# Optimization experiments

Measured on AMD Instinct MI355X. Metric: run time of the kernel, lower is better.

Reference implementation:

```python
import jax, jax.numpy as jnp
import numpy as np
from functools import partial

V, D, H, FF, NL, NC = 32000, 768, 12, 3072, 6, 1
B, L = 8, 512
EPS = 1e-5


def _layer_norm(x, g, b):
    m = jnp.mean(x, axis=-1, keepdims=True)
    v = jnp.mean((x - m) ** 2, axis=-1, keepdims=True)
    return (x - m) * jax.lax.rsqrt(v + EPS) * g + b


def setup_inputs() -> dict:
    key = jax.random.key(0)
    ks = jax.random.split(key, 24)
    s = 0.02
    inp = {
        'x': jax.random.randint(ks[0], (B, L), 0, V),
        'mask': jnp.ones((B, L), dtype=jnp.int32),
        'emb': jax.random.normal(ks[1], (V, D), jnp.float32) * s,
        # per-layer stacked params, leading dim = NL (scanned over)
        'Wq': jax.random.normal(ks[2], (NL, D, D), jnp.float32) * s,
        'bq': jnp.zeros((NL, D), jnp.float32),
        'Wk': jax.random.normal(ks[3], (NL, D, D), jnp.float32) * s,
        'bk': jnp.zeros((NL, D), jnp.float32),
        'Wv': jax.random.normal(ks[4], (NL, D, D), jnp.float32) * s,
        'bv': jnp.zeros((NL, D), jnp.float32),
        'Wo': jax.random.normal(ks[5], (NL, D, D), jnp.float32) * s,
        'bo': jnp.zeros((NL, D), jnp.float32),
        'W1': jax.random.normal(ks[6], (NL, D, FF), jnp.float32) * s,
        'b1': jnp.zeros((NL, FF), jnp.float32),
        'W2': jax.random.normal(ks[7], (NL, FF, D), jnp.float32) * s,
        'b2': jnp.zeros((NL, D), jnp.float32),
        'g1': jnp.ones((NL, D), jnp.float32),
        'be1': jnp.zeros((NL, D), jnp.float32),
        'g2': jnp.ones((NL, D), jnp.float32),
        'be2': jnp.zeros((NL, D), jnp.float32),
        'Wc': jax.random.normal(ks[8], (D, NC), jnp.float32) * s,
        'bc': jnp.zeros((NC,), jnp.float32),
    }
    return inp


def _forward(x, mask, emb, Wq, bq, Wk, bk, Wv, bv, Wo, bo, W1, b1, W2, b2,
             g1, be1, g2, be2, Wc, bc):
    Bx, Lx = x.shape
    Dm = emb.shape[1]
    dh = Dm // H
    scale = jnp.float32(np.sqrt(Dm / H))

    h = emb[x]  # [B,L,D]

    # PositionalEncoding (faithful to original buggy broadcast: pe[:B,0,:] added per-batch)
    pos = jnp.arange(Bx, dtype=jnp.float32)[:, None]
    div = jnp.exp(jnp.arange(0, Dm, 2, dtype=jnp.float32) * (-np.log(10000.0) / Dm))
    pe = jnp.stack([jnp.sin(pos * div), jnp.cos(pos * div)], axis=-1).reshape(Bx, Dm)
    h = h + pe[:, None, :]

    t = jnp.arange(Lx, dtype=jnp.float32)
    bias = -0.01 * (t[:, None] - t[None, :])  # [L,L]
    mask_b = (mask == 0)[:, None, None, :]    # [B,1,1,L]

    def step(h, p):
        (wq, bq_, wk, bk_, wv, bv_, wo, bo_, w1, b1_, w2, b2_,
         g1_, be1_, g2_, be2_) = p
        xn = _layer_norm(h, g1_, be1_)
        Q = (xn @ wq + bq_).reshape(Bx, Lx, H, dh)
        K = (xn @ wk + bk_).reshape(Bx, Lx, H, dh)
        Vv = (xn @ wv + bv_).reshape(Bx, Lx, H, dh)
        scores = jnp.einsum('bqhd,bkhd->bhqk', Q, K) / scale + bias
        scores = jnp.where(mask_b, -jnp.inf, scores)
        attn = jax.nn.softmax(scores, axis=-1)  # [B,H,L,L]
        out = jnp.einsum('bhqk,bkhd->bqhd', attn, Vv).reshape(Bx, Lx, Dm)
        h = h + (out @ wo + bo_)
        xn2 = _layer_norm(h, g2_, be2_)
        ff = jax.nn.gelu(xn2 @ w1 + b1_, approximate=False) @ w2 + b2_
        h = h + ff
        return h, attn

    params = (Wq, bq, Wk, bk, Wv, bv, Wo, bo, W1, b1, W2, b2, g1, be1, g2, be2)
    h, attn_all = jax.lax.scan(step, h, params)  # attn_all: [NL,B,H,L,L]
    logits = h[:, 0, :] @ Wc + bc  # CLS token -> [B,NC]
    return logits, attn_all


def reference(x, mask, emb, Wq, bq, Wk, bk, Wv, bv, Wo, bo, W1, b1, W2, b2,
              g1, be1, g2, be2, Wc, bc):
    return _forward(x, mask, emb, Wq, bq, Wk, bk, Wv, bv, Wo, bo,
                    W1, b1, W2, b2, g1, be1, g2, be2, Wc, bc)
```

## Files before the change

kernel.cpp:

```cpp
#include <hip/hip_runtime.h>
#include <math.h>

#define DMODEL 768
#define SEQL   512
#define NBATCH 8
#define NHEAD  12
#define NLAYER 6
#define FFDIM  3072
#define DHEAD  64
#define ROWS   (NBATCH * SEQL)
#define ATTN_PER_LAYER ((size_t)NBATCH * NHEAD * SEQL * SEQL)

using f32x4 = __attribute__((ext_vector_type(4))) float;
using f16x8 = __attribute__((ext_vector_type(8))) _Float16;
using f16x4 = __attribute__((ext_vector_type(4))) _Float16;

__device__ __forceinline__ void gload16(const void* g, void* l) {
    __builtin_amdgcn_global_load_lds(
        (const __attribute__((address_space(1))) unsigned int*)g,
        (__attribute__((address_space(3))) unsigned int*)l, 16, 0, 0);
}

__global__ __launch_bounds__(256) void embed_kernel(const int* __restrict__ x,
                                                    const float* __restrict__ emb,
                                                    float* __restrict__ h) {
    int bl = blockIdx.x;
    int b = bl >> 9;
    int tok = x[bl];
    const float* e = emb + (size_t)tok * DMODEL;
    float* hp = h + (size_t)bl * DMODEL;
    const float c = -0.011992632f;
#pragma unroll
    for (int u = 0; u < 3; ++u) {
        int d = threadIdx.x + u * 256;
        int i = d >> 1;
        float div = expf((float)(2 * i) * c);
        float ang = (float)b * div;
        float pe = (d & 1) ? cosf(ang) : sinf(ang);
        hp[d] = e[d] + pe;
    }
}

__global__ __launch_bounds__(256) void ln_kernel(const float* __restrict__ X,
                                                 const float* __restrict__ g,
                                                 const float* __restrict__ be,
                                                 _Float16* __restrict__ Yh,
                                                 _Float16* __restrict__ Yl) {
    int row = blockIdx.x;
    const float* x = X + (size_t)row * DMODEL;
    size_t base = (size_t)row * DMODEL;
    int t = threadIdx.x;
    float v0 = x[t], v1 = x[t + 256], v2 = x[t + 512];
    float s = v0 + v1 + v2;
    __shared__ float sb[8];
    for (int off = 32; off; off >>= 1) s += __shfl_down(s, off, 64);
    int lane = t & 63, wid = t >> 6;
    if (!lane) sb[wid] = s;
    __syncthreads();
    float mean = (sb[0] + sb[1] + sb[2] + sb[3]) * (1.0f / DMODEL);
    float d0 = v0 - mean, d1 = v1 - mean, d2 = v2 - mean;
    float q = d0 * d0 + d1 * d1 + d2 * d2;
    for (int off = 32; off; off >>= 1) q += __shfl_down(q, off, 64);
    if (!lane) sb[4 + wid] = q;
    __syncthreads();
    float var = (sb[4] + sb[5] + sb[6] + sb[7]) * (1.0f / DMODEL);
    float inv = 1.0f / sqrtf(var + 1e-5f);
    float y0 = d0 * inv * g[t] + be[t];
    float y1 = d1 * inv * g[t + 256] + be[t + 256];
    float y2 = d2 * inv * g[t + 512] + be[t + 512];
    _Float16 h0 = (_Float16)y0, h1 = (_Float16)y1, h2 = (_Float16)y2;
    Yh[base + t] = h0;       Yl[base + t] = (_Float16)(y0 - (float)h0);
    Yh[base + t + 256] = h1; Yl[base + t + 256] = (_Float16)(y1 - (float)h1);
    Yh[base + t + 512] = h2; Yl[base + t + 512] = (_Float16)(y2 - (float)h2);
}

__global__ __launch_bounds__(256) void wconv_kernel(const float* __restrict__ W,
                                                    _Float16* __restrict__ Th,
                                                    _Float16* __restrict__ Tl,
                                                    int K, int N) {
    __shared__ float t[32][33];
    int n0 = blockIdx.x * 32, k0 = blockIdx.y * 32;
    int tx = threadIdx.x & 31, ty = threadIdx.x >> 5;
#pragma unroll
    for (int u = 0; u < 4; ++u)
        t[ty + u * 8][tx] = W[(size_t)(k0 + ty + u * 8) * N + n0 + tx];
    __syncthreads();
#pragma unroll
    for (int u = 0; u < 4; ++u) {
        int r = ty + u * 8;
        float v = t[tx][r];
        _Float16 hi = (_Float16)v;
        size_t o = (size_t)(n0 + r) * K + k0 + tx;
        Th[o] = hi;
        Tl[o] = (_Float16)(v - (float)hi);
    }
}

__global__ __launch_bounds__(256) void fconv_kernel(const float* __restrict__ X,
                                                    _Float16* __restrict__ Xh,
                                                    _Float16* __restrict__ Xl,
                                                    int n4) {
    int i = blockIdx.x * 256 + threadIdx.x;
    if (i >= n4) return;
    float4 v = ((const float4*)X)[i];
    f16x4 hh, ll;
    hh[0] = (_Float16)v.x; ll[0] = (_Float16)(v.x - (float)hh[0]);
    hh[1] = (_Float16)v.y; ll[1] = (_Float16)(v.y - (float)hh[1]);
    hh[2] = (_Float16)v.z; ll[2] = (_Float16)(v.z - (float)hh[2]);
    hh[3] = (_Float16)v.w; ll[3] = (_Float16)(v.w - (float)hh[3]);
    ((f16x4*)Xh)[i] = hh;
    ((f16x4*)Xl)[i] = ll;
}

__global__ __launch_bounds__(256) void bcat_kernel(const float* __restrict__ a,
                                                   const float* __restrict__ b,
                                                   const float* __restrict__ c,
                                                   float* __restrict__ o) {
    int t = blockIdx.x * 256 + threadIdx.x;
    o[t] = (t < DMODEL) ? a[t] : (t < 2 * DMODEL ? b[t - DMODEL] : c[t - 2 * DMODEL]);
}

__global__ __launch_bounds__(256) void mgemm_kernel(
    const _Float16* __restrict__ Ah, const _Float16* __restrict__ Al,
    const _Float16* __restrict__ Bh, const _Float16* __restrict__ Bl,
    const float* __restrict__ bias, float* __restrict__ C,
    _Float16* __restrict__ Ch, _Float16* __restrict__ Cl,
    int N, int K, int flags) {
    __shared__ __attribute__((aligned(16))) _Float16 Ash[128][32];
    __shared__ __attribute__((aligned(16))) _Float16 Asl[128][32];
    __shared__ __attribute__((aligned(16))) _Float16 Bsh[128][32];
    __shared__ __attribute__((aligned(16))) _Float16 Bsl[128][32];

    int tid = threadIdx.x;
    int w = tid >> 6, lane = tid & 63;
    int m0 = blockIdx.y * 128, n0 = blockIdx.x * 128;
    int kper = K / gridDim.z;
    int kbeg = blockIdx.z * kper;

    int srow = lane >> 2;
    int kch = (lane & 3) ^ ((lane >> 3) & 3);
    size_t aoff0 = (size_t)(m0 + w * 16 + srow) * K + kch * 8;
    size_t aoff1 = (size_t)(m0 + (w + 4) * 16 + srow) * K + kch * 8;
    size_t boff0 = (size_t)(n0 + w * 16 + srow) * K + kch * 8;
    size_t boff1 = (size_t)(n0 + (w + 4) * 16 + srow) * K + kch * 8;
    _Float16* lAh0 = &Ash[w * 16][0];
    _Float16* lAh1 = &Ash[(w + 4) * 16][0];
    _Float16* lAl0 = &Asl[w * 16][0];
    _Float16* lAl1 = &Asl[(w + 4) * 16][0];
    _Float16* lBh0 = &Bsh[w * 16][0];
    _Float16* lBh1 = &Bsh[(w + 4) * 16][0];
    _Float16* lBl0 = &Bsl[w * 16][0];
    _Float16* lBl1 = &Bsl[(w + 4) * 16][0];

    int fr = lane & 15, kg = lane >> 4;
    int kb = (kg ^ ((fr >> 1) & 3)) * 8;
    int wr = w >> 1, wc = w & 1;

    f32x4 acc[4][4];
#pragma unroll
    for (int i = 0; i < 4; ++i)
#pragma unroll
        for (int j = 0; j < 4; ++j)
#pragma unroll
            for (int r = 0; r < 4; ++r) acc[i][j][r] = 0.0f;

    for (int k0 = kbeg; k0 < kbeg + kper; k0 += 32) {
        gload16(Ah + aoff0 + k0, lAh0);
        gload16(Ah + aoff1 + k0, lAh1);
        gload16(Al + aoff0 + k0, lAl0);
        gload16(Al + aoff1 + k0, lAl1);
        gload16(Bh + boff0 + k0, lBh0);
        gload16(Bh + boff1 + k0, lBh1);
        gload16(Bl + boff0 + k0, lBl0);
        gload16(Bl + boff1 + k0, lBl1);
        asm volatile("s_waitcnt vmcnt(0)" ::: "memory");
        __syncthreads();

        f16x8 a_h[4], a_l[4], b_h[4], b_l[4];
#pragma unroll
        for (int i = 0; i < 4; ++i) {
            int r = wr * 64 + i * 16 + fr;
            a_h[i] = *(const f16x8*)&Ash[r][kb];
            a_l[i] = *(const f16x8*)&Asl[r][kb];
        }
#pragma unroll
        for (int j = 0; j < 4; ++j) {
            int r = wc * 64 + j * 16 + fr;
            b_h[j] = *(const f16x8*)&Bsh[r][kb];
            b_l[j] = *(const f16x8*)&Bsl[r][kb];
        }
#pragma unroll
        for (int i = 0; i < 4; ++i)
#pragma unroll
            for (int j = 0; j < 4; ++j) {
                acc[i][j] = __builtin_amdgcn_mfma_f32_16x16x32_f16(a_h[i], b_h[j], acc[i][j], 0, 0, 0);
                acc[i][j] = __builtin_amdgcn_mfma_f32_16x16x32_f16(a_h[i], b_l[j], acc[i][j], 0, 0, 0);
                acc[i][j] = __builtin_amdgcn_mfma_f32_16x16x32_f16(a_l[i], b_h[j], acc[i][j], 0, 0, 0);
            }
        __syncthreads();
    }

    int od = kg * 4;
#pragma unroll
    for (int j = 0; j < 4; ++j) {
        int col = n0 + wc * 64 + j * 16 + fr;
        float bv = (bias && blockIdx.z == 0) ? bias[col] : 0.0f;
#pragma unroll
        for (int i = 0; i < 4; ++i) {
#pragma unroll
            for (int r = 0; r < 4; ++r) {
                int rowg = m0 + wr * 64 + i * 16 + od + r;
                float v = acc[i][j][r] + bv;
                if (flags & 1) v = 0.5f * v * (1.0f + erff(v * 0.70710678118654752f));
                size_t o = (size_t)rowg * N + col;
                if (flags & 4) {
                    _Float16 hv = (_Float16)v;
                    Ch[o] = hv;
                    Cl[o] = (_Float16)(v - (float)hv);
                } else if (flags & 2) {
                    unsafeAtomicAdd(&C[o], v);
                } else {
                    C[o] = v;
                }
            }
        }
    }
}

__global__ __launch_bounds__(256) void gemm_kernel(
    const float* __restrict__ A, const float* __restrict__ W,
    const float* __restrict__ bias, float* __restrict__ C,
    int M, int N, int K, int lda, int ldw, int ldc,
    int zmod, long long sAb, long long sAh, long long sWb, long long sWh,
    long long sCb, long long sCh, int flags) {
    int z = blockIdx.z;
    int zb = z / zmod, zh = z % zmod;
    A += zb * sAb + zh * sAh;
    W += zb * sWb + zh * sWh;
    C += zb * sCb + zh * sCh;

    __shared__ float As[16][65];
    __shared__ float Bs[16][64];
    int m0 = blockIdx.y * 64, n0 = blockIdx.x * 64;
    int tid = threadIdx.x;
    int tx = tid & 15, ty = tid >> 4;
    int arow = tid >> 2;
    int akk  = (tid & 3) << 2;
    int bkk  = tid >> 4;
    int bnn  = (tid & 15) << 2;
    float acc[4][4] = {};

    for (int k0 = 0; k0 < K; k0 += 16) {
        float4 av = *(const float4*)(A + (size_t)(m0 + arow) * lda + k0 + akk);
        float4 wv = *(const float4*)(W + (size_t)(k0 + bkk) * ldw + n0 + bnn);
        As[akk + 0][arow] = av.x;
        As[akk + 1][arow] = av.y;
        As[akk + 2][arow] = av.z;
        As[akk + 3][arow] = av.w;
        *(float4*)&Bs[bkk][bnn] = wv;
        __syncthreads();
#pragma unroll
        for (int k = 0; k < 16; ++k) {
            float a[4], bb[4];
#pragma unroll
            for (int i = 0; i < 4; ++i) a[i] = As[k][ty * 4 + i];
#pragma unroll
            for (int j = 0; j < 4; ++j) bb[j] = Bs[k][tx * 4 + j];
#pragma unroll
            for (int i = 0; i < 4; ++i)
#pragma unroll
                for (int j = 0; j < 4; ++j) acc[i][j] = fmaf(a[i], bb[j], acc[i][j]);
        }
        __syncthreads();
    }

#pragma unroll
    for (int i = 0; i < 4; ++i) {
        size_t rbase = (size_t)(m0 + ty * 4 + i) * ldc;
#pragma unroll
        for (int j = 0; j < 4; ++j) {
            int col = n0 + tx * 4 + j;
            float v = acc[i][j] + (bias ? bias[col] : 0.0f);
            if (flags & 1) v = 0.5f * v * (1.0f + erff(v * 0.70710678118654752f));
            if (flags & 2) C[rbase + col] += v;
            else           C[rbase + col] = v;
        }
    }
}

__global__ __launch_bounds__(256) void scores_kernel(const float* __restrict__ Q,
                                                     const float* __restrict__ Kmat,
                                                     const int* __restrict__ mask,
                                                     float* __restrict__ P,
                                                     int ldq) {
    int kt = blockIdx.x, qt = blockIdx.y, bh = blockIdx.z;
    int b = bh / NHEAD, hh = bh % NHEAD;
    int q0 = qt * 64, k0 = kt * 32;
    __shared__ float Qs[64][65];
    __shared__ float Ks[32][65];
    const float* Qg = Q + ((size_t)(b * SEQL + q0)) * ldq + hh * DHEAD;
    const float* Kg = Kmat + ((size_t)(b * SEQL + k0)) * ldq + hh * DHEAD;
    {
        int r = threadIdx.x >> 2;
        int c0 = (threadIdx.x & 3) * 16;
#pragma unroll
        for (int u = 0; u < 4; ++u) {
            float4 v = *(const float4*)(Qg + (size_t)r * ldq + c0 + u * 4);
            Qs[r][c0 + u * 4 + 0] = v.x;
            Qs[r][c0 + u * 4 + 1] = v.y;
            Qs[r][c0 + u * 4 + 2] = v.z;
            Qs[r][c0 + u * 4 + 3] = v.w;
        }
    }
    {
        int r = threadIdx.x >> 3;
        int c0 = (threadIdx.x & 7) * 8;
#pragma unroll
        for (int u = 0; u < 2; ++u) {
            float4 v = *(const float4*)(Kg + (size_t)r * ldq + c0 + u * 4);
            Ks[r][c0 + u * 4 + 0] = v.x;
            Ks[r][c0 + u * 4 + 1] = v.y;
            Ks[r][c0 + u * 4 + 2] = v.z;
            Ks[r][c0 + u * 4 + 3] = v.w;
        }
    }
    __syncthreads();
    int tq = threadIdx.x >> 3;
    int tk = threadIdx.x & 7;
    float acc[2][4] = {};
#pragma unroll 8
    for (int d = 0; d < 64; ++d) {
        float qa0 = Qs[tq * 2 + 0][d];
        float qa1 = Qs[tq * 2 + 1][d];
#pragma unroll
        for (int j = 0; j < 4; ++j) {
            float kb2 = Ks[tk * 4 + j][d];
            acc[0][j] = fmaf(qa0, kb2, acc[0][j]);
            acc[1][j] = fmaf(qa1, kb2, acc[1][j]);
        }
    }
    size_t pbase = ((size_t)(b * NHEAD + hh)) * SEQL;
#pragma unroll
    for (int i = 0; i < 2; ++i) {
        int qg = q0 + tq * 2 + i;
#pragma unroll
        for (int j = 0; j < 4; ++j) {
            int kg2 = k0 + tk * 4 + j;
            float v = acc[i][j] * 0.125f - 0.01f * ((float)qg - (float)kg2);
            if (mask[b * SEQL + kg2] == 0) v = -INFINITY;
            P[(pbase + qg) * SEQL + kg2] = v;
        }
    }
}

__global__ __launch_bounds__(256) void softmax_kernel(float* __restrict__ P) {
    int row = blockIdx.x * 4 + (threadIdx.x >> 6);
    int lane = threadIdx.x & 63;
    float* p = P + (size_t)row * SEQL;
    float v[8];
#pragma unroll
    for (int j = 0; j < 8; ++j) v[j] = p[lane + 64 * j];
    float m = v[0];
#pragma unroll
    for (int j = 1; j < 8; ++j) m = fmaxf(m, v[j]);
    for (int off = 32; off; off >>= 1) m = fmaxf(m, __shfl_xor(m, off, 64));
    float s = 0.0f;
#pragma unroll
    for (int j = 0; j < 8; ++j) {
        v[j] = expf(v[j] - m);
        s += v[j];
    }
    for (int off = 32; off; off >>= 1) s += __shfl_xor(s, off, 64);
    float inv = 1.0f / s;
#pragma unroll
    for (int j = 0; j < 8; ++j) p[lane + 64 * j] = v[j] * inv;
}

__global__ __launch_bounds__(256) void logits_kernel(const float* __restrict__ h,
                                                     const float* __restrict__ Wc,
                                                     const float* __restrict__ bc,
                                                     float* __restrict__ out) {
    int b = blockIdx.x;
    const float* hp = h + (size_t)b * SEQL * DMODEL;
    int t = threadIdx.x;
    float s = hp[t] * Wc[t] + hp[t + 256] * Wc[t + 256] + hp[t + 512] * Wc[t + 512];
    __shared__ float sb[4];
    for (int off = 32; off; off >>= 1) s += __shfl_down(s, off, 64);
    int lane = t & 63, wid = t >> 6;
    if (!lane) sb[wid] = s;
    __syncthreads();
    if (t == 0) out[b] = sb[0] + sb[1] + sb[2] + sb[3] + bc[0];
}

extern "C" void kernel_launch(void* const* d_in, const int* in_sizes, int n_in,
                              void* d_out, int out_size, void* d_ws, size_t ws_size,
                              hipStream_t stream) {
    (void)in_sizes; (void)n_in; (void)out_size; (void)ws_size;
    const int*   x    = (const int*)d_in[0];
    const int*   mask = (const int*)d_in[1];
    const float* emb  = (const float*)d_in[2];
    const float* Wq   = (const float*)d_in[3];
    const float* bq   = (const float*)d_in[4];
    const float* Wk   = (const float*)d_in[5];
    const float* bk   = (const float*)d_in[6];
    const float* Wv   = (const float*)d_in[7];
    const float* bv   = (const float*)d_in[8];
    const float* Wo   = (const float*)d_in[9];
    const float* bo   = (const float*)d_in[10];
    const float* W1   = (const float*)d_in[11];
    const float* b1   = (const float*)d_in[12];
    const float* W2   = (const float*)d_in[13];
    const float* b2   = (const float*)d_in[14];
    const float* g1   = (const float*)d_in[15];
    const float* be1  = (const float*)d_in[16];
    const float* g2   = (const float*)d_in[17];
    const float* be2  = (const float*)d_in[18];
    const float* Wc   = (const float*)d_in[19];
    const float* bc   = (const float*)d_in[20];

    float* out  = (float*)d_out;
    float* attn = out + NBATCH * 1;

    const size_t RD  = (size_t)ROWS * DMODEL;
    const size_t RFF = (size_t)ROWS * FFDIM;
    const size_t DD  = (size_t)DMODEL * DMODEL;
    const size_t DF  = (size_t)DMODEL * FFDIM;

    float* ws   = (float*)d_ws;
    float* h    = ws;
    float* qkvb = h + RD;
    float* att  = qkvb + 3 * RD;
    _Float16* xnh  = (_Float16*)(att + RD);
    _Float16* xnl  = xnh + RD;
    _Float16* atth = xnl + RD;
    _Float16* attl = atth + RD;
    _Float16* ffh  = attl + RD;
    _Float16* ffl  = ffh + RFF;
    _Float16* wqkvh = ffl + RFF;
    _Float16* wqkvl = wqkvh + 3 * DD;
    _Float16* woh  = wqkvl + 3 * DD;
    _Float16* wol  = woh + DD;
    _Float16* w1h  = wol + DD;
    _Float16* w1l  = w1h + DF;
    _Float16* w2h  = w1l + DF;
    _Float16* w2l  = w2h + DF;
    float* bqkv = (float*)(w2l + DF);

    embed_kernel<<<ROWS, 256, 0, stream>>>(x, emb, h);

    for (int l = 0; l < NLAYER; ++l) {
        const float* wq = Wq + (size_t)l * DD;
        const float* wk = Wk + (size_t)l * DD;
        const float* wv = Wv + (size_t)l * DD;
        const float* wo = Wo + (size_t)l * DD;
        const float* w1 = W1 + (size_t)l * DF;
        const float* w2 = W2 + (size_t)l * DF;
        float* P = attn + (size_t)l * ATTN_PER_LAYER;

        wconv_kernel<<<dim3(24, 24), 256, 0, stream>>>(wq, wqkvh,          wqkvl,          DMODEL, DMODEL);
        wconv_kernel<<<dim3(24, 24), 256, 0, stream>>>(wk, wqkvh + DD,     wqkvl + DD,     DMODEL, DMODEL);
        wconv_kernel<<<dim3(24, 24), 256, 0, stream>>>(wv, wqkvh + 2 * DD, wqkvl + 2 * DD, DMODEL, DMODEL);
        wconv_kernel<<<dim3(24, 24), 256, 0, stream>>>(wo, woh, wol, DMODEL, DMODEL);
        wconv_kernel<<<dim3(96, 24), 256, 0, stream>>>(w1, w1h, w1l, DMODEL, FFDIM);
        wconv_kernel<<<dim3(24, 96), 256, 0, stream>>>(w2, w2h, w2l, FFDIM, DMODEL);
        bcat_kernel<<<9, 256, 0, stream>>>(bq + l * DMODEL, bk + l * DMODEL, bv + l * DMODEL, bqkv);

        ln_kernel<<<ROWS, 256, 0, stream>>>(h, g1 + l * DMODEL, be1 + l * DMODEL, xnh, xnl);

        mgemm_kernel<<<dim3(18, 32, 1), 256, 0, stream>>>(
            xnh, xnl, wqkvh, wqkvl, bqkv, qkvb, nullptr, nullptr,
            3 * DMODEL, DMODEL, 0);

        scores_kernel<<<dim3(SEQL / 32, SEQL / 64, NBATCH * NHEAD), 256, 0, stream>>>(
            qkvb, qkvb + DMODEL, mask, P, 3 * DMODEL);
        softmax_kernel<<<(NBATCH * NHEAD * SEQL) / 4, 256, 0, stream>>>(P);

        gemm_kernel<<<dim3(1, SEQL / 64, NBATCH * NHEAD), 256, 0, stream>>>(
            P, qkvb + 2 * DMODEL, nullptr, att,
            SEQL, DHEAD, SEQL, SEQL, 3 * DMODEL, DMODEL,
            NHEAD,
            (long long)NHEAD * SEQL * SEQL, (long long)SEQL * SEQL,
            (long long)SEQL * 3 * DMODEL, (long long)DHEAD,
            (long long)SEQL * DMODEL, (long long)DHEAD, 0);

        fconv_kernel<<<(int)(RD / 4 / 256), 256, 0, stream>>>(att, atth, attl, (int)(RD / 4));

        mgemm_kernel<<<dim3(6, 32, 2), 256, 0, stream>>>(
            atth, attl, woh, wol, bo + l * DMODEL, h, nullptr, nullptr,
            DMODEL, DMODEL, 2);

        ln_kernel<<<ROWS, 256, 0, stream>>>(h, g2 + l * DMODEL, be2 + l * DMODEL, xnh, xnl);

        mgemm_kernel<<<dim3(24, 32, 1), 256, 0, stream>>>(
            xnh, xnl, w1h, w1l, b1 + l * FFDIM, nullptr, ffh, ffl,
            FFDIM, DMODEL, 1 | 4);

        mgemm_kernel<<<dim3(6, 32, 4), 256, 0, stream>>>(
            ffh, ffl, w2h, w2l, b2 + l * DMODEL, h, nullptr, nullptr,
            DMODEL, FFDIM, 2);
    }

    logits_kernel<<<NBATCH, 256, 0, stream>>>(h, Wc, bc, out);
}
```

Baseline: 3.717 ms.

## Fuse QK scores with softmax and move attention onto split-fp16 MFMA

Replaces the scalar fp32 scores, softmax and PV GEMM kernels with MFMA-based kernels using hi/lo fp16 splitting. The QKV projection now emits fp16 hi/lo pairs directly. Scores, bias, mask and softmax are fused into one kernel that holds a full 512-wide row block in registers and writes P once, instead of writing and rereading it. A V-transpose kernel feeds a PV kernel that also emits hi/lo fp16 output, which removes the separate conversion pass. The split-fp16 scheme risks small accuracy differences, and 32 f32x4 accumulators per lane put pressure on registers.

```diff
diff --git a/kernel.cpp b/kernel.cpp
--- a/kernel.cpp
+++ b/kernel.cpp
@@ -96,28 +96,200 @@
     }
 }
 
-__global__ __launch_bounds__(256) void fconv_kernel(const float* __restrict__ X,
-                                                    _Float16* __restrict__ Xh,
-                                                    _Float16* __restrict__ Xl,
-                                                    int n4) {
-    int i = blockIdx.x * 256 + threadIdx.x;
-    if (i >= n4) return;
-    float4 v = ((const float4*)X)[i];
-    f16x4 hh, ll;
-    hh[0] = (_Float16)v.x; ll[0] = (_Float16)(v.x - (float)hh[0]);
-    hh[1] = (_Float16)v.y; ll[1] = (_Float16)(v.y - (float)hh[1]);
-    hh[2] = (_Float16)v.z; ll[2] = (_Float16)(v.z - (float)hh[2]);
-    hh[3] = (_Float16)v.w; ll[3] = (_Float16)(v.w - (float)hh[3]);
-    ((f16x4*)Xh)[i] = hh;
-    ((f16x4*)Xl)[i] = ll;
-}
-
 __global__ __launch_bounds__(256) void bcat_kernel(const float* __restrict__ a,
                                                    const float* __restrict__ b,
                                                    const float* __restrict__ c,
                                                    float* __restrict__ o) {
     int t = blockIdx.x * 256 + threadIdx.x;
     o[t] = (t < DMODEL) ? a[t] : (t < 2 * DMODEL ? b[t - DMODEL] : c[t - 2 * DMODEL]);
+}
+
+__global__ __launch_bounds__(256) void vtrans_kernel(const _Float16* __restrict__ Vh,
+                                                     const _Float16* __restrict__ Vl,
+                                                     _Float16* __restrict__ Oh,
+                                                     _Float16* __restrict__ Ol) {
+    int kt = blockIdx.x, bh = blockIdx.y;
+    int b = bh / NHEAD, hh = bh % NHEAD;
+    int k0 = kt * 64;
+    __shared__ _Float16 th[64][68];
+    __shared__ _Float16 tl[64][68];
+    int t = threadIdx.x;
+    int r = t >> 2, c0 = (t & 3) * 16;
+    size_t src = (size_t)(b * SEQL + k0 + r) * 2304 + 1536 + hh * DHEAD + c0;
+#pragma unroll
+    for (int u = 0; u < 4; ++u) {
+        *(f16x4*)&th[r][c0 + u * 4] = *(const f16x4*)(Vh + src + u * 4);
+        *(f16x4*)&tl[r][c0 + u * 4] = *(const f16x4*)(Vl + src + u * 4);
+    }
+    __syncthreads();
+    int d = t >> 2, q4 = t & 3;
+    size_t dst = ((size_t)bh * 64 + d) * SEQL + k0;
+#pragma unroll
+    for (int u = 0; u < 4; ++u) {
+        int klo = (q4 + u * 4) * 4;
+        f16x4 a, bb;
+#pragma unroll
+        for (int j = 0; j < 4; ++j) { a[j] = th[klo + j][d]; bb[j] = tl[klo + j][d]; }
+        *(f16x4*)(Oh + dst + klo) = a;
+        *(f16x4*)(Ol + dst + klo) = bb;
+    }
+}
+
+__global__ __launch_bounds__(256) void attn_kernel(const _Float16* __restrict__ QKh,
+                                                   const _Float16* __restrict__ QKl,
+                                                   const int* __restrict__ mask,
+                                                   float* __restrict__ P) {
+    int qt = blockIdx.x, bh = blockIdx.y;
+    int b = bh / NHEAD, hh = bh % NHEAD;
+    int w = threadIdx.x >> 6, lane = threadIdx.x & 63;
+    int fr = lane & 15, kg = lane >> 4;
+    int q0 = qt * 64 + w * 16;
+
+    __shared__ int msk[SEQL];
+    msk[threadIdx.x] = mask[b * SEQL + threadIdx.x];
+    msk[threadIdx.x + 256] = mask[b * SEQL + threadIdx.x + 256];
+    __syncthreads();
+
+    const _Float16* qrh = QKh + (size_t)(b * SEQL + q0 + fr) * 2304 + hh * DHEAD;
+    const _Float16* qrl = QKl + (size_t)(b * SEQL + q0 + fr) * 2304 + hh * DHEAD;
+    f16x8 ah0 = *(const f16x8*)(qrh + kg * 8);
+    f16x8 ah1 = *(const f16x8*)(qrh + 32 + kg * 8);
+    f16x8 al0 = *(const f16x8*)(qrl + kg * 8);
+    f16x8 al1 = *(const f16x8*)(qrl + 32 + kg * 8);
+
+    f32x4 acc[32];
+#pragma unroll
+    for (int nt = 0; nt < 32; ++nt)
+#pragma unroll
+        for (int r = 0; r < 4; ++r) acc[nt][r] = 0.0f;
+
+    const _Float16* kbh = QKh + (size_t)(b * SEQL) * 2304 + DMODEL + hh * DHEAD;
+    const _Float16* kbl = QKl + (size_t)(b * SEQL) * 2304 + DMODEL + hh * DHEAD;
+#pragma unroll
+    for (int nt = 0; nt < 32; ++nt) {
+        const _Float16* krh = kbh + (size_t)(nt * 16 + fr) * 2304;
+        const _Float16* krl = kbl + (size_t)(nt * 16 + fr) * 2304;
+        f16x8 bh0 = *(const f16x8*)(krh + kg * 8);
+        f16x8 bh1 = *(const f16x8*)(krh + 32 + kg * 8);
+        f16x8 bl0 = *(const f16x8*)(krl + kg * 8);
+        f16x8 bl1 = *(const f16x8*)(krl + 32 + kg * 8);
+        f32x4 a = acc[nt];
+        a = __builtin_amdgcn_mfma_f32_16x16x32_f16(ah0, bh0, a, 0, 0, 0);
+        a = __builtin_amdgcn_mfma_f32_16x16x32_f16(ah1, bh1, a, 0, 0, 0);
+        a = __builtin_amdgcn_mfma_f32_16x16x32_f16(ah0, bl0, a, 0, 0, 0);
+        a = __builtin_amdgcn_mfma_f32_16x16x32_f16(ah1, bl1, a, 0, 0, 0);
+        a = __builtin_amdgcn_mfma_f32_16x16x32_f16(al0, bh0, a, 0, 0, 0);
+        a = __builtin_amdgcn_mfma_f32_16x16x32_f16(al1, bh1, a, 0, 0, 0);
+        acc[nt] = a;
+    }
+
+    float mx[4] = {-INFINITY, -INFINITY, -INFINITY, -INFINITY};
+#pragma unroll
+    for (int nt = 0; nt < 32; ++nt) {
+        int k = nt * 16 + fr;
+        float bk = 0.01f * (float)k;
+        bool dead = (msk[k] == 0);
+#pragma unroll
+        for (int r = 0; r < 4; ++r) {
+            float s = acc[nt][r] * 0.125f - 0.01f * (float)(q0 + kg * 4 + r) + bk;
+            if (dead) s = -INFINITY;
+            acc[nt][r] = s;
+            mx[r] = fmaxf(mx[r], s);
+        }
+    }
+    float sm[4];
+#pragma unroll
+    for (int r = 0; r < 4; ++r) {
+        float m = mx[r];
+        m = fmaxf(m, __shfl_xor(m, 1, 64));
+        m = fmaxf(m, __shfl_xor(m, 2, 64));
+        m = fmaxf(m, __shfl_xor(m, 4, 64));
+        m = fmaxf(m, __shfl_xor(m, 8, 64));
+        mx[r] = m;
+        sm[r] = 0.0f;
+    }
+#pragma unroll
+    for (int nt = 0; nt < 32; ++nt)
+#pragma unroll
+        for (int r = 0; r < 4; ++r) {
+            float e = expf(acc[nt][r] - mx[r]);
+            acc[nt][r] = e;
+            sm[r] += e;
+        }
+#pragma unroll
+    for (int r = 0; r < 4; ++r) {
+        float s = sm[r];
+        s += __shfl_xor(s, 1, 64);
+        s += __shfl_xor(s, 2, 64);
+        s += __shfl_xor(s, 4, 64);
+        s += __shfl_xor(s, 8, 64);
+        sm[r] = 1.0f / s;
+    }
+    float* prow = P + ((size_t)bh * SEQL + q0 + kg * 4) * SEQL + fr;
+#pragma unroll
+    for (int r = 0; r < 4; ++r)
+#pragma unroll
+        for (int nt = 0; nt < 32; ++nt)
+            prow[(size_t)r * SEQL + nt * 16] = acc[nt][r] * sm[r];
+}
+
+__global__ __launch_bounds__(256) void pv_kernel(const float* __restrict__ P,
+                                                 const _Float16* __restrict__ Vth,
+                                                 const _Float16* __restrict__ Vtl,
+                                                 _Float16* __restrict__ Oh,
+                                                 _Float16* __restrict__ Ol) {
+    int qt = blockIdx.x, bh = blockIdx.y;
+    int b = bh / NHEAD, hh = bh % NHEAD;
+    int w = threadIdx.x >> 6, lane = threadIdx.x & 63;
+    int fr = lane & 15, kg = lane >> 4;
+    int q0 = qt * 64 + w * 16;
+
+    const float* prow = P + ((size_t)bh * SEQL + q0 + fr) * SEQL + kg * 8;
+    const _Float16* vbh[4];
+    const _Float16* vbl[4];
+#pragma unroll
+    for (int nf = 0; nf < 4; ++nf) {
+        size_t o = ((size_t)bh * 64 + nf * 16 + fr) * SEQL + kg * 8;
+        vbh[nf] = Vth + o;
+        vbl[nf] = Vtl + o;
+    }
+    f32x4 acc[4];
+#pragma unroll
+    for (int nf = 0; nf < 4; ++nf)
+#pragma unroll
+        for (int r = 0; r < 4; ++r) acc[nf][r] = 0.0f;
+
+#pragma unroll
+    for (int ks = 0; ks < 16; ++ks) {
+        float4 p0 = *(const float4*)(prow + ks * 32);
+        float4 p1 = *(const float4*)(prow + ks * 32 + 4);
+        float pv[8] = {p0.x, p0.y, p0.z, p0.w, p1.x, p1.y, p1.z, p1.w};
+        f16x8 ph, pl;
+#pragma unroll
+        for (int e = 0; e < 8; ++e) {
+            _Float16 hv = (_Float16)pv[e];
+            ph[e] = hv;
+            pl[e] = (_Float16)(pv[e] - (float)hv);
+        }
+#pragma unroll
+        for (int nf = 0; nf < 4; ++nf) {
+            f16x8 vh = *(const f16x8*)(vbh[nf] + ks * 32);
+            f16x8 vl = *(const f16x8*)(vbl[nf] + ks * 32);
+            acc[nf] = __builtin_amdgcn_mfma_f32_16x16x32_f16(ph, vh, acc[nf], 0, 0, 0);
+            acc[nf] = __builtin_amdgcn_mfma_f32_16x16x32_f16(ph, vl, acc[nf], 0, 0, 0);
+            acc[nf] = __builtin_amdgcn_mfma_f32_16x16x32_f16(pl, vh, acc[nf], 0, 0, 0);
+        }
+    }
+#pragma unroll
+    for (int nf = 0; nf < 4; ++nf)
+#pragma unroll
+        for (int r = 0; r < 4; ++r) {
+            size_t o = (size_t)(b * SEQL + q0 + kg * 4 + r) * DMODEL + hh * DHEAD + nf * 16 + fr;
+            float v = acc[nf][r];
+            _Float16 hv = (_Float16)v;
+            Oh[o] = hv;
+            Ol[o] = (_Float16)(v - (float)hv);
+        }
 }
 
 __global__ __launch_bounds__(256) void mgemm_kernel(
@@ -225,155 +397,6 @@
             }
         }
     }
-}
-
-__global__ __launch_bounds__(256) void gemm_kernel(
-    const float* __restrict__ A, const float* __restrict__ W,
-    const float* __restrict__ bias, float* __restrict__ C,
-    int M, int N, int K, int lda, int ldw, int ldc,
-    int zmod, long long sAb, long long sAh, long long sWb, long long sWh,
-    long long sCb, long long sCh, int flags) {
-    int z = blockIdx.z;
-    int zb = z / zmod, zh = z % zmod;
-    A += zb * sAb + zh * sAh;
-    W += zb * sWb + zh * sWh;
-    C += zb * sCb + zh * sCh;
-
-    __shared__ float As[16][65];
-    __shared__ float Bs[16][64];
-    int m0 = blockIdx.y * 64, n0 = blockIdx.x * 64;
-    int tid = threadIdx.x;
-    int tx = tid & 15, ty = tid >> 4;
-    int arow = tid >> 2;
-    int akk  = (tid & 3) << 2;
-    int bkk  = tid >> 4;
-    int bnn  = (tid & 15) << 2;
-    float acc[4][4] = {};
-
-    for (int k0 = 0; k0 < K; k0 += 16) {
-        float4 av = *(const float4*)(A + (size_t)(m0 + arow) * lda + k0 + akk);
-        float4 wv = *(const float4*)(W + (size_t)(k0 + bkk) * ldw + n0 + bnn);
-        As[akk + 0][arow] = av.x;
-        As[akk + 1][arow] = av.y;
-        As[akk + 2][arow] = av.z;
-        As[akk + 3][arow] = av.w;
-        *(float4*)&Bs[bkk][bnn] = wv;
-        __syncthreads();
-#pragma unroll
-        for (int k = 0; k < 16; ++k) {
-            float a[4], bb[4];
-#pragma unroll
-            for (int i = 0; i < 4; ++i) a[i] = As[k][ty * 4 + i];
-#pragma unroll
-            for (int j = 0; j < 4; ++j) bb[j] = Bs[k][tx * 4 + j];
-#pragma unroll
-            for (int i = 0; i < 4; ++i)
-#pragma unroll
-                for (int j = 0; j < 4; ++j) acc[i][j] = fmaf(a[i], bb[j], acc[i][j]);
-        }
-        __syncthreads();
-    }
-
-#pragma unroll
-    for (int i = 0; i < 4; ++i) {
-        size_t rbase = (size_t)(m0 + ty * 4 + i) * ldc;
-#pragma unroll
-        for (int j = 0; j < 4; ++j) {
-            int col = n0 + tx * 4 + j;
-            float v = acc[i][j] + (bias ? bias[col] : 0.0f);
-            if (flags & 1) v = 0.5f * v * (1.0f + erff(v * 0.70710678118654752f));
-            if (flags & 2) C[rbase + col] += v;
-            else           C[rbase + col] = v;
-        }
-    }
-}
-
-__global__ __launch_bounds__(256) void scores_kernel(const float* __restrict__ Q,
-                                                     const float* __restrict__ Kmat,
-                                                     const int* __restrict__ mask,
-                                                     float* __restrict__ P,
-                                                     int ldq) {
-    int kt = blockIdx.x, qt = blockIdx.y, bh = blockIdx.z;
-    int b = bh / NHEAD, hh = bh % NHEAD;
-    int q0 = qt * 64, k0 = kt * 32;
-    __shared__ float Qs[64][65];
-    __shared__ float Ks[32][65];
-    const float* Qg = Q + ((size_t)(b * SEQL + q0)) * ldq + hh * DHEAD;
-    const float* Kg = Kmat + ((size_t)(b * SEQL + k0)) * ldq + hh * DHEAD;
-    {
-        int r = threadIdx.x >> 2;
-        int c0 = (threadIdx.x & 3) * 16;
-#pragma unroll
-        for (int u = 0; u < 4; ++u) {
-            float4 v = *(const float4*)(Qg + (size_t)r * ldq + c0 + u * 4);
-            Qs[r][c0 + u * 4 + 0] = v.x;
-            Qs[r][c0 + u * 4 + 1] = v.y;
-            Qs[r][c0 + u * 4 + 2] = v.z;
-            Qs[r][c0 + u * 4 + 3] = v.w;
-        }
-    }
-    {
-        int r = threadIdx.x >> 3;
-        int c0 = (threadIdx.x & 7) * 8;
-#pragma unroll
-        for (int u = 0; u < 2; ++u) {
-            float4 v = *(const float4*)(Kg + (size_t)r * ldq + c0 + u * 4);
-            Ks[r][c0 + u * 4 + 0] = v.x;
-            Ks[r][c0 + u * 4 + 1] = v.y;
-            Ks[r][c0 + u * 4 + 2] = v.z;
-            Ks[r][c0 + u * 4 + 3] = v.w;
-        }
-    }
-    __syncthreads();
-    int tq = threadIdx.x >> 3;
-    int tk = threadIdx.x & 7;
-    float acc[2][4] = {};
-#pragma unroll 8
-    for (int d = 0; d < 64; ++d) {
-        float qa0 = Qs[tq * 2 + 0][d];
-        float qa1 = Qs[tq * 2 + 1][d];
-#pragma unroll
-        for (int j = 0; j < 4; ++j) {
-            float kb2 = Ks[tk * 4 + j][d];
-            acc[0][j] = fmaf(qa0, kb2, acc[0][j]);
-            acc[1][j] = fmaf(qa1, kb2, acc[1][j]);
-        }
-    }
-    size_t pbase = ((size_t)(b * NHEAD + hh)) * SEQL;
-#pragma unroll
-    for (int i = 0; i < 2; ++i) {
-        int qg = q0 + tq * 2 + i;
-#pragma unroll
-        for (int j = 0; j < 4; ++j) {
-            int kg2 = k0 + tk * 4 + j;
-            float v = acc[i][j] * 0.125f - 0.01f * ((float)qg - (float)kg2);
-            if (mask[b * SEQL + kg2] == 0) v = -INFINITY;
-            P[(pbase + qg) * SEQL + kg2] = v;
-        }
-    }
-}
-
-__global__ __launch_bounds__(256) void softmax_kernel(float* __restrict__ P) {
-    int row = blockIdx.x * 4 + (threadIdx.x >> 6);
-    int lane = threadIdx.x & 63;
-    float* p = P + (size_t)row * SEQL;
-    float v[8];
-#pragma unroll
-    for (int j = 0; j < 8; ++j) v[j] = p[lane + 64 * j];
-    float m = v[0];
-#pragma unroll
-    for (int j = 1; j < 8; ++j) m = fmaxf(m, v[j]);
-    for (int off = 32; off; off >>= 1) m = fmaxf(m, __shfl_xor(m, off, 64));
-    float s = 0.0f;
-#pragma unroll
-    for (int j = 0; j < 8; ++j) {
-        v[j] = expf(v[j] - m);
-        s += v[j];
-    }
-    for (int off = 32; off; off >>= 1) s += __shfl_xor(s, off, 64);
-    float inv = 1.0f / s;
-#pragma unroll
-    for (int j = 0; j < 8; ++j) p[lane + 64 * j] = v[j] * inv;
 }
 
 __global__ __launch_bounds__(256) void logits_kernel(const float* __restrict__ h,
@@ -428,11 +451,13 @@
 
     float* ws   = (float*)d_ws;
     float* h    = ws;
-    float* qkvb = h + RD;
-    float* att  = qkvb + 3 * RD;
-    _Float16* xnh  = (_Float16*)(att + RD);
+    _Float16* xnh  = (_Float16*)(h + RD);
     _Float16* xnl  = xnh + RD;
-    _Float16* atth = xnl + RD;
+    _Float16* qkvh = xnl + RD;
+    _Float16* qkvl = qkvh + 3 * RD;
+    _Float16* vth  = qkvl + 3 * RD;
+    _Float16* vtl  = vth + RD;
+    _Float16* atth = vtl + RD;
     _Float16* attl = atth + RD;
     _Float16* ffh  = attl + RD;
     _Float16* ffl  = ffh + RFF;
@@ -468,22 +493,17 @@
         ln_kernel<<<ROWS, 256, 0, stream>>>(h, g1 + l * DMODEL, be1 + l * DMODEL, xnh, xnl);
 
         mgemm_kernel<<<dim3(18, 32, 1), 256, 0, stream>>>(
-            xnh, xnl, wqkvh, wqkvl, bqkv, qkvb, nullptr, nullptr,
-            3 * DMODEL, DMODEL, 0);
-
-        scores_kernel<<<dim3(SEQL / 32, SEQL / 64, NBATCH * NHEAD), 256, 0, stream>>>(
-            qkvb, qkvb + DMODEL, mask, P, 3 * DMODEL);
-        softmax_kernel<<<(NBATCH * NHEAD * SEQL) / 4, 256, 0, stream>>>(P);
-
-        gemm_kernel<<<dim3(1, SEQL / 64, NBATCH * NHEAD), 256, 0, stream>>>(
-            P, qkvb + 2 * DMODEL, nullptr, att,
-            SEQL, DHEAD, SEQL, SEQL, 3 * DMODEL, DMODEL,
-            NHEAD,
-            (long long)NHEAD * SEQL * SEQL, (long long)SEQL * SEQL,
-            (long long)SEQL * 3 * DMODEL, (long long)DHEAD,
-            (long long)SEQL * DMODEL, (long long)DHEAD, 0);
-
-        fconv_kernel<<<(int)(RD / 4 / 256), 256, 0, stream>>>(att, atth, attl, (int)(RD / 4));
+            xnh, xnl, wqkvh, wqkvl, bqkv, nullptr, qkvh, qkvl,
+            3 * DMODEL, DMODEL, 4);
+
+        vtrans_kernel<<<dim3(SEQL / 64, NBATCH * NHEAD), 256, 0, stream>>>(
+            qkvh, qkvl, vth, vtl);
+
+        attn_kernel<<<dim3(SEQL / 64, NBATCH * NHEAD), 256, 0, stream>>>(
+            qkvh, qkvl, mask, P);
+
+        pv_kernel<<<dim3(SEQL / 64, NBATCH * NHEAD), 256, 0, stream>>>(
+            P, vth, vtl, atth, attl);
 
         mgemm_kernel<<<dim3(6, 32, 2), 256, 0, stream>>>(
             atth, attl, woh, wol, bo + l * DMODEL, h, nullptr, nullptr,
```

Result: no change. 3.681 ms (-1.0%).
